# Optimization experiments

Hardware: AMD Instinct MI355X
Metric: run time of the kernel (lower is better)

## Reference

```python
import jax, jax.numpy as jnp
import numpy as np

COST_CLASS, COST_BBOX, COST_GIOU = 1.0, 5.0, 2.0
NUM_FRAMES, Q_PER_FRAME, NUM_TGT, NUM_CLASSES = 36, 100, 20, 92
B = 64


def box_cxcywh_to_xyxy(b):
    cx, cy, w, h = b[..., 0], b[..., 1], b[..., 2], b[..., 3]
    return jnp.stack([cx - 0.5 * w, cy - 0.5 * h, cx + 0.5 * w, cy + 0.5 * h], axis=-1)


def pairwise_giou(b1, b2):
    # b1: [..., Q, 4], b2: [..., T, 4], xyxy -> giou [..., Q, T]
    area1 = (b1[..., 2] - b1[..., 0]) * (b1[..., 3] - b1[..., 1])
    area2 = (b2[..., 2] - b2[..., 0]) * (b2[..., 3] - b2[..., 1])
    lt = jnp.maximum(b1[..., :, None, :2], b2[..., None, :, :2])
    rb = jnp.minimum(b1[..., :, None, 2:], b2[..., None, :, 2:])
    wh = jnp.clip(rb - lt, 0.0)
    inter = wh[..., 0] * wh[..., 1]
    union = area1[..., :, None] + area2[..., None, :] - inter
    iou = inter / union
    lt_e = jnp.minimum(b1[..., :, None, :2], b2[..., None, :, :2])
    rb_e = jnp.maximum(b1[..., :, None, 2:], b2[..., None, :, 2:])
    wh_e = jnp.clip(rb_e - lt_e, 0.0)
    area_e = wh_e[..., 0] * wh_e[..., 1]
    return iou - (area_e - union) / area_e


def compute_cost(pred_logits, pred_boxes, tgt_labels, tgt_boxes):
    b = pred_logits.shape[0]
    prob = jax.nn.softmax(pred_logits.reshape(b, NUM_FRAMES, Q_PER_FRAME, -1), axis=-1)  # [B,F,Q,C]
    pb = pred_boxes.reshape(b, NUM_FRAMES, Q_PER_FRAME, 4)
    lab = jnp.transpose(tgt_labels, (1, 0, 2))            # [B,F,T]
    tb = jnp.transpose(tgt_boxes, (1, 0, 2, 3))           # [B,F,T,4]
    onehot = jax.nn.one_hot(lab, prob.shape[-1], dtype=prob.dtype)  # [B,F,T,C]
    cost_class = -jnp.einsum('bfqc,bftc->bfqt', prob, onehot)
    cost_bbox = jnp.abs(pb[:, :, :, None, :] - tb[:, :, None, :, :]).sum(-1)  # L1 cdist
    giou = pairwise_giou(box_cxcywh_to_xyxy(pb), box_cxcywh_to_xyxy(tb))
    return COST_CLASS * cost_class + COST_BBOX * cost_bbox - COST_GIOU * giou


def auction_assign(cost):
    # cost [Q, T]; returns obj_of [T]: query index assigned to each target.
    # eps-optimal auction algorithm (replaces scipy linear_sum_assignment).
    Q, T = cost.shape
    benefit = -cost.T  # [T, Q]
    spread = jnp.max(benefit) - jnp.min(benefit) + 1e-6
    eps = spread / 1000.0
    neg_inf = jnp.asarray(-1e30, cost.dtype)

    def cond(s):
        _, _, obj_of, it = s
        return jnp.logical_and(jnp.any(obj_of < 0), it < 20000)

    def body(s):
        price, owner, obj_of, it = s
        unassigned = obj_of < 0                       # [T]
        vals = benefit - price[None, :]               # [T, Q]
        top2v, top2i = jax.lax.top_k(vals, 2)
        best_obj = top2i[:, 0]                        # [T]
        bid = price[best_obj] + (top2v[:, 0] - top2v[:, 1]) + eps
        bid = jnp.where(unassigned, bid, neg_inf)
        best_bid = jnp.full((Q,), neg_inf, cost.dtype).at[best_obj].max(bid)
        pids = jnp.arange(T, dtype=jnp.int32)
        win = unassigned & (bid >= best_bid[best_obj])
        winner = jnp.full((Q,), T, jnp.int32).at[best_obj].min(jnp.where(win, pids, T))
        has_bid = winner < T
        # evict previous owners of objects that received a bid
        evict = jnp.where(has_bid & (owner >= 0), owner, T)
        obj_of = obj_of.at[evict].set(-1, mode='drop')
        qids = jnp.arange(Q, dtype=jnp.int32)
        obj_of = obj_of.at[jnp.where(has_bid, winner, T)].set(jnp.where(has_bid, qids, -1), mode='drop')
        price = jnp.where(has_bid, best_bid, price)
        owner = jnp.where(has_bid, winner, owner)
        return price, owner, obj_of, it + 1

    init = (jnp.zeros((Q,), cost.dtype), jnp.full((Q,), -1, jnp.int32),
            jnp.full((T,), -1, jnp.int32), jnp.int32(0))
    _, _, obj_of, _ = jax.lax.while_loop(cond, body, init)
    return obj_of


def setup_inputs() -> dict:
    key = jax.random.key(0)
    k1, k2, k3, k4 = jax.random.split(key, 4)
    pred_logits = jax.random.normal(k1, (B, NUM_FRAMES * Q_PER_FRAME, NUM_CLASSES), jnp.float32)
    pred_boxes = jax.random.uniform(k2, (B, NUM_FRAMES * Q_PER_FRAME, 4), jnp.float32)
    tgt_labels = jax.random.randint(k3, (NUM_FRAMES, B, NUM_TGT), 0, NUM_CLASSES, jnp.int32)
    tgt_boxes = jax.random.uniform(k4, (NUM_FRAMES, B, NUM_TGT, 4), jnp.float32)
    return {'pred_logits': pred_logits, 'pred_boxes': pred_boxes,
            'tgt_labels': tgt_labels, 'tgt_boxes': tgt_boxes}


def reference(pred_logits, pred_boxes, tgt_labels, tgt_boxes):
    cost = compute_cost(pred_logits, pred_boxes, tgt_labels, tgt_boxes)  # [B,F,Q,T]
    b, f, q, t = cost.shape
    obj_of = jax.vmap(auction_assign)(cost.reshape(b * f, q, t))  # [BF, T]
    order = jnp.argsort(obj_of, axis=-1)  # scipy returns rows ascending
    pred_idx = jnp.take_along_axis(obj_of, order, axis=-1).reshape(b, f, t)
    tgt_idx = order.astype(jnp.int32).reshape(b, f, t)
    return cost, pred_idx, tgt_idx
```

## Files before the change

kernel.cpp:

```cpp
#include <hip/hip_runtime.h>

#define NF 36
#define QN 100
#define TN 20
#define CN 92
#define NB 64

__global__ __launch_bounds__(128) void matcher_kernel(
    const float* __restrict__ logits,
    const float* __restrict__ pboxes,
    const int*   __restrict__ tlabels,
    const float* __restrict__ tboxes,
    float* __restrict__ out_cost,
    float* __restrict__ out_pred,
    float* __restrict__ out_tgt)
{
    const int bf = blockIdx.x;
    const int b  = bf / NF;
    const int f  = bf % NF;
    const int tid = threadIdx.x;

    __shared__ float ben[TN][101];
    __shared__ float price[QN];
    __shared__ int   owner[QN];
    __shared__ int   obj_of[TN];
    __shared__ float bidv[TN];
    __shared__ int   bo[TN];
    __shared__ float bb[QN];
    __shared__ int   win[QN];
    __shared__ float pv0[100], pv1[100];
    __shared__ int   pi0[100];
    __shared__ int   slab[TN];
    __shared__ float tbr[TN][4];
    __shared__ float tbx[TN][4];
    __shared__ float tarea[TN];
    __shared__ float rmin[128], rmax[128];
    __shared__ float s_eps;
    __shared__ int   s_un;

    if (tid < TN) {
        const int base = (f * NB + b) * TN + tid;
        slab[tid] = tlabels[base];
        const float* tb = tboxes + (size_t)base * 4;
        float cx = tb[0], cy = tb[1], w = tb[2], h = tb[3];
        tbr[tid][0] = cx; tbr[tid][1] = cy; tbr[tid][2] = w; tbr[tid][3] = h;
        float x1 = cx - 0.5f * w, y1 = cy - 0.5f * h;
        float x2 = cx + 0.5f * w, y2 = cy + 0.5f * h;
        tbx[tid][0] = x1; tbx[tid][1] = y1; tbx[tid][2] = x2; tbx[tid][3] = y2;
        tarea[tid] = (x2 - x1) * (y2 - y1);
        obj_of[tid] = -1;
    }
    if (tid < QN) { price[tid] = 0.f; owner[tid] = -1; }
    if (tid == 0) s_un = TN;
    float lmin = INFINITY, lmax = -INFINITY;
    __syncthreads();

    if (tid < QN) {
        const size_t row = (size_t)b * (NF * QN) + (size_t)f * QN + tid;
        const float* L = logits + row * CN;
        const float4* L4 = reinterpret_cast<const float4*>(L);
        float m = -INFINITY;
        #pragma unroll
        for (int i = 0; i < CN / 4; ++i) {
            float4 v = L4[i];
            m = fmaxf(m, v.x); m = fmaxf(m, v.y); m = fmaxf(m, v.z); m = fmaxf(m, v.w);
        }
        float s = 0.f;
        #pragma unroll
        for (int i = 0; i < CN / 4; ++i) {
            float4 v = L4[i];
            s += expf(v.x - m); s += expf(v.y - m); s += expf(v.z - m); s += expf(v.w - m);
        }

        const float* pb = pboxes + row * 4;
        float cx = pb[0], cy = pb[1], w = pb[2], h = pb[3];
        float px1 = cx - 0.5f * w, py1 = cy - 0.5f * h;
        float px2 = cx + 0.5f * w, py2 = cy + 0.5f * h;
        float a1 = (px2 - px1) * (py2 - py1);

        for (int t = 0; t < TN; ++t) {
            float p = expf(L[slab[t]] - m) / s;
            float cb = fabsf(cx - tbr[t][0]) + fabsf(cy - tbr[t][1]);
            cb = cb + fabsf(w - tbr[t][2]);
            cb = cb + fabsf(h - tbr[t][3]);
            float ltx = fmaxf(px1, tbx[t][0]), lty = fmaxf(py1, tbx[t][1]);
            float rbx = fminf(px2, tbx[t][2]), rby = fminf(py2, tbx[t][3]);
            float wx = fmaxf(rbx - ltx, 0.f), wy = fmaxf(rby - lty, 0.f);
            float inter = wx * wy;
            float uni = a1 + tarea[t] - inter;
            float iou = inter / uni;
            float ex1 = fminf(px1, tbx[t][0]), ey1 = fminf(py1, tbx[t][1]);
            float ex2 = fmaxf(px2, tbx[t][2]), ey2 = fmaxf(py2, tbx[t][3]);
            float ew = fmaxf(ex2 - ex1, 0.f), eh = fmaxf(ey2 - ey1, 0.f);
            float ae = ew * eh;
            float giou = iou - (ae - uni) / ae;
            float cost = (-p) + 5.0f * cb - 2.0f * giou;
            ben[t][tid] = -cost;
            lmin = fminf(lmin, cost);
            lmax = fmaxf(lmax, cost);
        }
    }
    rmin[tid] = lmin; rmax[tid] = lmax;
    __syncthreads();

    {
        float4* dst = reinterpret_cast<float4*>(out_cost + (size_t)bf * (QN * TN));
        for (int i = tid; i < (QN * TN) / 4; i += 128) {
            int k = i * 4;
            float4 v;
            v.x = -ben[(k + 0) % TN][(k + 0) / TN];
            v.y = -ben[(k + 1) % TN][(k + 1) / TN];
            v.z = -ben[(k + 2) % TN][(k + 2) / TN];
            v.w = -ben[(k + 3) % TN][(k + 3) / TN];
            dst[i] = v;
        }
    }
    if (tid == 0) {
        float mn = INFINITY, mx = -INFINITY;
        for (int i = 0; i < 128; ++i) { mn = fminf(mn, rmin[i]); mx = fmaxf(mx, rmax[i]); }
        float spread = (-mn) - (-mx) + 1e-6f;
        s_eps = spread / 1000.0f;
    }

    for (int it = 0; it < 20000; ++it) {
        __syncthreads();
        if (s_un == 0) break;

        if (tid < 100) {
            int t = tid / 5, j = tid % 5;
            if (obj_of[t] < 0) {
                int q0 = j * 20;
                float v0 = -INFINITY, v1 = -INFINITY; int i0 = q0;
                const float* rowp = ben[t];
                #pragma unroll
                for (int q = q0; q < q0 + 20; ++q) {
                    float v = rowp[q] - price[q];
                    if (v > v0) { v1 = v0; v0 = v; i0 = q; }
                    else if (v > v1) { v1 = v; }
                }
                pv0[tid] = v0; pv1[tid] = v1; pi0[tid] = i0;
            }
        }
        __syncthreads();

        if (tid < TN) {
            if (obj_of[tid] < 0) {
                int base = tid * 5;
                float v0 = pv0[base], v1 = pv1[base]; int i0 = pi0[base];
                #pragma unroll
                for (int j = 1; j < 5; ++j) {
                    float bv0 = pv0[base + j], bv1 = pv1[base + j]; int bi0 = pi0[base + j];
                    if (bv0 > v0) { v1 = fmaxf(v0, bv1); v0 = bv0; i0 = bi0; }
                    else          { v1 = fmaxf(bv0, v1); }
                }
                bidv[tid] = price[i0] + (v0 - v1) + s_eps;
                bo[tid] = i0;
            } else {
                bidv[tid] = -INFINITY;
            }
        }
        __syncthreads();

        if (tid < QN) {
            float best = -INFINITY; int wt = TN;
            #pragma unroll
            for (int t = 0; t < TN; ++t) {
                float bd = bidv[t];
                if (bd != -INFINITY && bo[t] == tid && bd > best) { best = bd; wt = t; }
            }
            bb[tid] = best; win[tid] = wt;
        }
        __syncthreads();

        if (tid < TN) {
            float bd = bidv[tid];
            if (bd != -INFINITY) {
                int q = bo[tid];
                if (win[q] == tid) {
                    int old = owner[q];
                    if (old >= 0) { obj_of[old] = -1; atomicAdd(&s_un, 1); }
                    obj_of[tid] = q;
                    owner[q] = tid;
                    price[q] = bb[q];
                    atomicSub(&s_un, 1);
                }
            }
        }
    }
    __syncthreads();

    if (tid < TN) {
        int v = obj_of[tid];
        int r = 0;
        for (int u = 0; u < TN; ++u) {
            int w = obj_of[u];
            r += (w < v) || (w == v && u < tid);
        }
        out_pred[(size_t)bf * TN + r] = (float)v;
        out_tgt[(size_t)bf * TN + r]  = (float)tid;
    }
}

extern "C" void kernel_launch(void* const* d_in, const int* in_sizes, int n_in,
                              void* d_out, int out_size, void* d_ws, size_t ws_size,
                              hipStream_t stream) {
    const float* logits  = (const float*)d_in[0];
    const float* pboxes  = (const float*)d_in[1];
    const int*   tlabels = (const int*)d_in[2];
    const float* tboxes  = (const float*)d_in[3];

    float* out = (float*)d_out;
    float* out_cost = out;
    float* out_pred = out + (size_t)NB * NF * QN * TN;
    float* out_tgt  = out_pred + (size_t)NB * NF * TN;

    dim3 grid(NB * NF);
    dim3 block(128);
    hipLaunchKernelGGL(matcher_kernel, grid, block, 0, stream,
                       logits, pboxes, tlabels, tboxes, out_cost, out_pred, out_tgt);
}
```

Baseline: 211.2 us.

## Split matcher into cost kernel and single-wavefront auction kernel

Result: slower. 246.5 us (+16.7%).

```diff
diff --git a/kernel.cpp b/kernel.cpp
--- a/kernel.cpp
+++ b/kernel.cpp
@@ -5,38 +5,26 @@
 #define TN 20
 #define CN 92
 #define NB 64
-
-__global__ __launch_bounds__(128) void matcher_kernel(
+#define LSTRIDE 93
+
+__global__ __launch_bounds__(128) void cost_kernel(
     const float* __restrict__ logits,
     const float* __restrict__ pboxes,
     const int*   __restrict__ tlabels,
     const float* __restrict__ tboxes,
-    float* __restrict__ out_cost,
-    float* __restrict__ out_pred,
-    float* __restrict__ out_tgt)
+    float* __restrict__ out_cost)
 {
     const int bf = blockIdx.x;
     const int b  = bf / NF;
     const int f  = bf % NF;
     const int tid = threadIdx.x;
 
+    __shared__ float Llds[QN * LSTRIDE];
     __shared__ float ben[TN][101];
-    __shared__ float price[QN];
-    __shared__ int   owner[QN];
-    __shared__ int   obj_of[TN];
-    __shared__ float bidv[TN];
-    __shared__ int   bo[TN];
-    __shared__ float bb[QN];
-    __shared__ int   win[QN];
-    __shared__ float pv0[100], pv1[100];
-    __shared__ int   pi0[100];
     __shared__ int   slab[TN];
     __shared__ float tbr[TN][4];
     __shared__ float tbx[TN][4];
     __shared__ float tarea[TN];
-    __shared__ float rmin[128], rmax[128];
-    __shared__ float s_eps;
-    __shared__ int   s_un;
 
     if (tid < TN) {
         const int base = (f * NB + b) * TN + tid;
@@ -48,32 +36,31 @@
         float x2 = cx + 0.5f * w, y2 = cy + 0.5f * h;
         tbx[tid][0] = x1; tbx[tid][1] = y1; tbx[tid][2] = x2; tbx[tid][3] = y2;
         tarea[tid] = (x2 - x1) * (y2 - y1);
-        obj_of[tid] = -1;
-    }
-    if (tid < QN) { price[tid] = 0.f; owner[tid] = -1; }
-    if (tid == 0) s_un = TN;
-    float lmin = INFINITY, lmax = -INFINITY;
+    }
+
+    {
+        const float4* G4 = reinterpret_cast<const float4*>(
+            logits + ((size_t)b * (NF * QN) + (size_t)f * QN) * CN);
+        for (int i = tid; i < (QN * CN) / 4; i += 128) {
+            float4 v = G4[i];
+            int row = i / 23;
+            int col = (i - row * 23) * 4;
+            float* dst = &Llds[row * LSTRIDE + col];
+            dst[0] = v.x; dst[1] = v.y; dst[2] = v.z; dst[3] = v.w;
+        }
+    }
     __syncthreads();
 
     if (tid < QN) {
+        const float* L = &Llds[tid * LSTRIDE];
+        float m = -INFINITY;
+        for (int c = 0; c < CN; ++c) m = fmaxf(m, L[c]);
+        float s = 0.f;
+        for (int c = 0; c < CN; ++c) s += expf(L[c] - m);
+
         const size_t row = (size_t)b * (NF * QN) + (size_t)f * QN + tid;
-        const float* L = logits + row * CN;
-        const float4* L4 = reinterpret_cast<const float4*>(L);
-        float m = -INFINITY;
-        #pragma unroll
-        for (int i = 0; i < CN / 4; ++i) {
-            float4 v = L4[i];
-            m = fmaxf(m, v.x); m = fmaxf(m, v.y); m = fmaxf(m, v.z); m = fmaxf(m, v.w);
-        }
-        float s = 0.f;
-        #pragma unroll
-        for (int i = 0; i < CN / 4; ++i) {
-            float4 v = L4[i];
-            s += expf(v.x - m); s += expf(v.y - m); s += expf(v.z - m); s += expf(v.w - m);
-        }
-
-        const float* pb = pboxes + row * 4;
-        float cx = pb[0], cy = pb[1], w = pb[2], h = pb[3];
+        float4 pbv = reinterpret_cast<const float4*>(pboxes)[row];
+        float cx = pbv.x, cy = pbv.y, w = pbv.z, h = pbv.w;
         float px1 = cx - 0.5f * w, py1 = cy - 0.5f * h;
         float px2 = cx + 0.5f * w, py2 = cy + 0.5f * h;
         float a1 = (px2 - px1) * (py2 - py1);
@@ -96,11 +83,8 @@
             float giou = iou - (ae - uni) / ae;
             float cost = (-p) + 5.0f * cb - 2.0f * giou;
             ben[t][tid] = -cost;
-            lmin = fminf(lmin, cost);
-            lmax = fmaxf(lmax, cost);
-        }
-    }
-    rmin[tid] = lmin; rmax[tid] = lmax;
+        }
+    }
     __syncthreads();
 
     {
@@ -115,89 +99,124 @@
             dst[i] = v;
         }
     }
-    if (tid == 0) {
-        float mn = INFINITY, mx = -INFINITY;
-        for (int i = 0; i < 128; ++i) { mn = fminf(mn, rmin[i]); mx = fmaxf(mx, rmax[i]); }
-        float spread = (-mn) - (-mx) + 1e-6f;
-        s_eps = spread / 1000.0f;
-    }
+}
+
+__global__ __launch_bounds__(64) void auction_kernel(
+    const float* __restrict__ cost_in,
+    float* __restrict__ out_pred,
+    float* __restrict__ out_tgt)
+{
+    const int bf = blockIdx.x;
+    const int lane = threadIdx.x;
+
+    __shared__ float ben[TN][101];
+    __shared__ float price[QN];
+    __shared__ int   owner[QN];
+    __shared__ int   obj_of[TN];
+    __shared__ float pv0[64], pv1[64];
+    __shared__ int   pi0[64];
+    __shared__ float bidv[TN];
+    __shared__ int   bo[TN];
+
+    float mn = INFINITY, mx = -INFINITY;
+    {
+        const float4* C4 = reinterpret_cast<const float4*>(cost_in + (size_t)bf * (QN * TN));
+        #pragma unroll
+        for (int k = 0; k < 8; ++k) {
+            int i = lane + 64 * k;
+            if (i < (QN * TN) / 4) {
+                float4 v = C4[i];
+                int q  = i / 5;
+                int t0 = (i - q * 5) * 4;
+                ben[t0 + 0][q] = -v.x; ben[t0 + 1][q] = -v.y;
+                ben[t0 + 2][q] = -v.z; ben[t0 + 3][q] = -v.w;
+                mn = fminf(mn, fminf(fminf(v.x, v.y), fminf(v.z, v.w)));
+                mx = fmaxf(mx, fmaxf(fmaxf(v.x, v.y), fmaxf(v.z, v.w)));
+            }
+        }
+    }
+    #pragma unroll
+    for (int off = 32; off > 0; off >>= 1) {
+        mn = fminf(mn, __shfl_xor(mn, off, 64));
+        mx = fmaxf(mx, __shfl_xor(mx, off, 64));
+    }
+    const float eps = (((-mn) - (-mx)) + 1e-6f) / 1000.0f;
+
+    if (lane < QN) { price[lane] = 0.f; owner[lane] = -1; }
+    if (lane + 64 < QN) { price[lane + 64] = 0.f; owner[lane + 64] = -1; }
+    if (lane < TN) obj_of[lane] = -1;
 
     for (int it = 0; it < 20000; ++it) {
         __syncthreads();
-        if (s_un == 0) break;
-
-        if (tid < 100) {
-            int t = tid / 5, j = tid % 5;
+        unsigned long long un = __ballot((lane < TN) ? (obj_of[lane] < 0) : false);
+        if (un == 0ull) break;
+
+        if (lane < 60) {
+            int t = lane / 3, j = lane - t * 3;
             if (obj_of[t] < 0) {
-                int q0 = j * 20;
+                const float* rowp = ben[t];
+                int q0 = j * 34;
                 float v0 = -INFINITY, v1 = -INFINITY; int i0 = q0;
-                const float* rowp = ben[t];
                 #pragma unroll
-                for (int q = q0; q < q0 + 20; ++q) {
-                    float v = rowp[q] - price[q];
-                    if (v > v0) { v1 = v0; v0 = v; i0 = q; }
-                    else if (v > v1) { v1 = v; }
+                for (int k = 0; k < 34; ++k) {
+                    int q = q0 + k;
+                    if (q < QN) {
+                        float v = rowp[q] - price[q];
+                        if (v > v0) { v1 = v0; v0 = v; i0 = q; }
+                        else if (v > v1) { v1 = v; }
+                    }
                 }
-                pv0[tid] = v0; pv1[tid] = v1; pi0[tid] = i0;
+                pv0[lane] = v0; pv1[lane] = v1; pi0[lane] = i0;
             }
         }
         __syncthreads();
 
-        if (tid < TN) {
-            if (obj_of[tid] < 0) {
-                int base = tid * 5;
+        float mybid = -INFINITY; int myq = -1;
+        if (lane < TN) {
+            if (obj_of[lane] < 0) {
+                int base = lane * 3;
                 float v0 = pv0[base], v1 = pv1[base]; int i0 = pi0[base];
                 #pragma unroll
-                for (int j = 1; j < 5; ++j) {
+                for (int j = 1; j < 3; ++j) {
                     float bv0 = pv0[base + j], bv1 = pv1[base + j]; int bi0 = pi0[base + j];
                     if (bv0 > v0) { v1 = fmaxf(v0, bv1); v0 = bv0; i0 = bi0; }
                     else          { v1 = fmaxf(bv0, v1); }
                 }
-                bidv[tid] = price[i0] + (v0 - v1) + s_eps;
-                bo[tid] = i0;
-            } else {
-                bidv[tid] = -INFINITY;
-            }
+                mybid = price[i0] + (v0 - v1) + eps;
+                myq = i0;
+            }
+            bidv[lane] = mybid; bo[lane] = myq;
         }
         __syncthreads();
 
-        if (tid < QN) {
-            float best = -INFINITY; int wt = TN;
+        if (lane < TN && mybid != -INFINITY) {
+            bool lose = false;
             #pragma unroll
-            for (int t = 0; t < TN; ++t) {
-                float bd = bidv[t];
-                if (bd != -INFINITY && bo[t] == tid && bd > best) { best = bd; wt = t; }
-            }
-            bb[tid] = best; win[tid] = wt;
-        }
-        __syncthreads();
-
-        if (tid < TN) {
-            float bd = bidv[tid];
-            if (bd != -INFINITY) {
-                int q = bo[tid];
-                if (win[q] == tid) {
-                    int old = owner[q];
-                    if (old >= 0) { obj_of[old] = -1; atomicAdd(&s_un, 1); }
-                    obj_of[tid] = q;
-                    owner[q] = tid;
-                    price[q] = bb[q];
-                    atomicSub(&s_un, 1);
-                }
+            for (int t2 = 0; t2 < TN; ++t2) {
+                float bv = bidv[t2]; int ob = bo[t2];
+                lose = lose || (ob == myq && (bv > mybid || (bv == mybid && t2 < lane)));
+            }
+            if (!lose) {
+                int q = myq;
+                int old = owner[q];
+                if (old >= 0) obj_of[old] = -1;
+                obj_of[lane] = q;
+                owner[q] = lane;
+                price[q] = mybid;
             }
         }
     }
     __syncthreads();
 
-    if (tid < TN) {
-        int v = obj_of[tid];
+    if (lane < TN) {
+        int v = obj_of[lane];
         int r = 0;
         for (int u = 0; u < TN; ++u) {
             int w = obj_of[u];
-            r += (w < v) || (w == v && u < tid);
+            r += (w < v) || (w == v && u < lane);
         }
         out_pred[(size_t)bf * TN + r] = (float)v;
-        out_tgt[(size_t)bf * TN + r]  = (float)tid;
+        out_tgt[(size_t)bf * TN + r]  = (float)lane;
     }
 }
 
@@ -214,8 +233,8 @@
     float* out_pred = out + (size_t)NB * NF * QN * TN;
     float* out_tgt  = out_pred + (size_t)NB * NF * TN;
 
-    dim3 grid(NB * NF);
-    dim3 block(128);
-    hipLaunchKernelGGL(matcher_kernel, grid, block, 0, stream,
-                       logits, pboxes, tlabels, tboxes, out_cost, out_pred, out_tgt);
+    hipLaunchKernelGGL(cost_kernel, dim3(NB * NF), dim3(128), 0, stream,
+                       logits, pboxes, tlabels, tboxes, out_cost);
+    hipLaunchKernelGGL(auction_kernel, dim3(NB * NF), dim3(64), 0, stream,
+                       out_cost, out_pred, out_tgt);
 }
```
